# Optimization experiments

Hardware: AMD Instinct MI355X
Metric: run time of the kernel (lower is better)

Reference implementation:

```python
import jax, jax.numpy as jnp
import numpy as np

N = 1048576  # batch elements; each element is a 64-bit FP64 value stored as {0,1} float bits


def _xor(a, b):
    return a + b - 2.0 * a * b


def _mux(s, a, b):
    # s ? a : b  (spiking MUX gate)
    return s * a + (1.0 - s) * b


def _ripple_add(a, b, c0):
    """Bitwise ripple-carry add of little-endian bit vectors a,b [..., n] with carry-in c0 [...]."""
    def step(carry, ab):
        ai, bi = ab
        x = _xor(ai, bi)
        s = _xor(x, carry)
        c = ai * bi + carry * x - ai * bi * carry * x  # OR(a&b, c&(a^b))
        return c, s
    _, sums = jax.lax.scan(step, c0, (jnp.moveaxis(a, -1, 0), jnp.moveaxis(b, -1, 0)))
    return jnp.moveaxis(sums, 0, -1)


def setup_inputs() -> dict:
    key = jax.random.key(0)
    kx, kk = jax.random.split(key)
    x = jax.random.randint(kx, (N, 64), 0, 2).astype(jnp.float32)
    k = jax.random.randint(kk, (N, 64), 0, 2).astype(jnp.float32)
    return {"x": x, "k": k}


def reference(x, k):
    batch = x.shape[:-1]
    dt = x.dtype
    ones = jnp.ones(batch, dt)
    zeros = jnp.zeros(batch, dt)

    s_x = x[..., 0:1]
    e_x = x[..., 1:12]
    m_x = x[..., 12:64]
    s_k = k[..., 0:1]
    e_k = k[..., 1:12]
    m_k = k[..., 12:64]

    # shift = e_k - 1023 (little-endian, two's complement via add of NOT(1023)+1)
    e_k_le = e_k[..., ::-1]
    not_1023_le = jnp.broadcast_to(jnp.asarray([0.0] * 10 + [1.0], dt), batch + (11,))
    shift = _ripple_add(e_k_le, not_1023_le, ones)

    # barrel shifter: integer value of |k| = (1.mantissa) >> (15 - shift)  over 16 bits
    s_bar = 1.0 - shift[..., :4]  # bits of (15 - shift)
    val = jnp.concatenate([jnp.ones(batch + (1,), dt), m_k[..., :15]], axis=-1)
    current = val[..., ::-1]  # little-endian
    for layer in range(4):
        amt = 1 << layer
        shifted = jnp.concatenate([current[..., amt:], jnp.zeros(batch + (amt,), dt)], axis=-1)
        current = _mux(s_bar[..., layer:layer + 1], shifted, current)
    k_abs_le = current[..., :11]

    # negate via two's complement; select by sign of k
    neg_k = _ripple_add(1.0 - k_abs_le, jnp.zeros(batch + (11,), dt), ones)
    k_final = _mux(s_k, neg_k, k_abs_le)

    # e_new = e_x + k_final
    e_x_le = e_x[..., ::-1]
    e_new = _ripple_add(e_x_le, k_final, zeros)[..., ::-1]

    # k == 0 detection: OR-reduce bits 1..63 (OR(a,b)=1-(1-a)(1-b)), then NOT
    k_is_zero = jnp.prod(1.0 - k[..., 1:64], axis=-1, keepdims=True)

    result_scaled = jnp.concatenate([s_x, e_new, m_x], axis=-1)
    return _mux(k_is_zero, x, result_scaled)
```

## Files before the change

### kernel.cpp

```cpp
#include <hip/hip_runtime.h>


typedef unsigned int u32x4 __attribute__((ext_vector_type(4)));

__global__ __launch_bounds__(256) void spike_fp64_scale_kernel(
    const u32x4* __restrict__ x4,
    const u32x4* __restrict__ k4,
    u32x4* __restrict__ o4,
    int ntiles)
{
    const int nwaves = (int)((gridDim.x * blockDim.x) >> 6);
    const int wid    = (int)((blockIdx.x * blockDim.x + threadIdx.x) >> 6);
    const int lane   = (int)(threadIdx.x & 63);
    const int g      = lane >> 4;
    const int j      = lane & 15;

    if (wid >= ntiles) return;

    size_t idx        = (size_t)wid * 64 + lane;
    const size_t step = (size_t)nwaves * 64;

    u32x4 xv = x4[idx];
    u32x4 kv = k4[idx];

    int tile = wid;
    for (;;) {
        const int  nxt      = tile + nwaves;
        const bool has_next = nxt < ntiles;
        u32x4 xn, kn;
        if (has_next) {
            xn = x4[idx + step];
            kn = k4[idx + step];
        }

        const unsigned nx = ((xv[0] >> 23) & 1u) | ((xv[1] >> 22) & 2u)
                          | ((xv[2] >> 21) & 4u) | ((xv[3] >> 20) & 8u);
        const unsigned nk = ((kv[0] >> 23) & 1u) | ((kv[1] >> 22) & 2u)
                          | ((kv[2] >> 21) & 4u) | ((kv[3] >> 20) & 8u);

        const unsigned sh4 = (unsigned)(j & 7) * 4u;
        unsigned uxl = (j < 8) ? (nx << sh4) : 0u;
        unsigned ukl = (j < 8) ? (nk << sh4) : 0u;

        const unsigned nkm = nk & ((j == 0) ? 0xEu : 0xFu);
        const unsigned long long bal = __ballot(nkm != 0u);
        const bool kany = ((unsigned)((bal >> (g * 16)) & 0xFFFFull)) != 0u;

        #pragma unroll
        for (int m = 1; m <= 8; m <<= 1) {
            uxl |= (unsigned)__shfl_xor((int)uxl, m, 64);
            ukl |= (unsigned)__shfl_xor((int)ukl, m, 64);
        }

        const unsigned bk    = __builtin_bitreverse32(ukl);
        const unsigned ek    = (bk >> 20) & 0x7FFu;
        const unsigned val16 = 0x8000u | ((bk >> 5) & 0x7FFFu);
        const unsigned shv   = (ek + 1u) & 15u;
        const unsigned kabs  = (val16 >> (15u - shv)) & 0x7FFu;
        const unsigned kfin  = (ukl & 1u) ? ((0u - kabs) & 0x7FFu) : kabs;
        const unsigned ex    = (__builtin_bitreverse32(uxl) >> 20) & 0x7FFu;
        const unsigned enew  = (ex + kfin) & 0x7FFu;

        u32x4 o;
        const int e0 = 4 * j;
        #pragma unroll
        for (int c = 0; c < 4; ++c) {
            const int e = e0 + c;
            const unsigned bit  = (enew >> (((unsigned)(11 - e)) & 31u)) & 1u;
            const bool     repl = kany && (e >= 1) && (e <= 11);
            o[c] = repl ? (bit ? 0x3F800000u : 0u) : xv[c];
        }
        __builtin_nontemporal_store(o, &o4[idx]);

        if (!has_next) break;
        tile = nxt;
        idx += step;
        xv = xn;
        kv = kn;
    }
}

extern "C" void kernel_launch(void* const* d_in, const int* in_sizes, int n_in,
                              void* d_out, int out_size, void* d_ws, size_t ws_size,
                              hipStream_t stream) {
    const u32x4* x4 = (const u32x4*)d_in[0];
    const u32x4* k4 = (const u32x4*)d_in[1];
    u32x4* o4 = (u32x4*)d_out;

    const int nrows  = in_sizes[0] / 64;
    const int ntiles = nrows / 4;

    const int threads = 256;
    int blocks = 2048;
    const int max_blocks = (ntiles * 64 + threads - 1) / threads;
    if (blocks > max_blocks) blocks = max_blocks;

    spike_fp64_scale_kernel<<<blocks, threads, 0, stream>>>(x4, k4, o4, ntiles);
}
```

Measured before the change: 602.2 us.

## Replace grid-stride prefetch loop with one-tile-per-wave launch and DPP reductions

After: 564.3 us. -6.3%, faster.

```diff
diff --git a/kernel.cpp b/kernel.cpp
--- a/kernel.cpp
+++ b/kernel.cpp
@@ -3,81 +3,59 @@
 
 typedef unsigned int u32x4 __attribute__((ext_vector_type(4)));
 
+#define DPP_OR(v, ctrl) \
+    (v | (unsigned)__builtin_amdgcn_update_dpp(0, (int)(v), (ctrl), 0xF, 0xF, true))
+
 __global__ __launch_bounds__(256) void spike_fp64_scale_kernel(
     const u32x4* __restrict__ x4,
     const u32x4* __restrict__ k4,
-    u32x4* __restrict__ o4,
-    int ntiles)
+    u32x4* __restrict__ o4)
 {
-    const int nwaves = (int)((gridDim.x * blockDim.x) >> 6);
-    const int wid    = (int)((blockIdx.x * blockDim.x + threadIdx.x) >> 6);
-    const int lane   = (int)(threadIdx.x & 63);
-    const int g      = lane >> 4;
-    const int j      = lane & 15;
+    const int lane = (int)(threadIdx.x & 63);
+    const int g    = lane >> 4;
+    const int j    = lane & 15;
 
-    if (wid >= ntiles) return;
+    const size_t idx = (size_t)((blockIdx.x * blockDim.x + threadIdx.x) >> 6) * 64 + lane;
+    const u32x4 xv = x4[idx];
+    const u32x4 kv = k4[idx];
 
-    size_t idx        = (size_t)wid * 64 + lane;
-    const size_t step = (size_t)nwaves * 64;
+    const unsigned nx = ((xv[0] >> 23) & 1u) | ((xv[1] >> 22) & 2u)
+                      | ((xv[2] >> 21) & 4u) | ((xv[3] >> 20) & 8u);
+    const unsigned nk = ((kv[0] >> 23) & 1u) | ((kv[1] >> 22) & 2u)
+                      | ((kv[2] >> 21) & 4u) | ((kv[3] >> 20) & 8u);
 
-    u32x4 xv = x4[idx];
-    u32x4 kv = k4[idx];
+    const unsigned sh4 = (unsigned)(j & 7) * 4u;
+    unsigned uxl = (j < 8) ? (nx << sh4) : 0u;
+    unsigned ukl = (j < 8) ? (nk << sh4) : 0u;
 
-    int tile = wid;
-    for (;;) {
-        const int  nxt      = tile + nwaves;
-        const bool has_next = nxt < ntiles;
-        u32x4 xn, kn;
-        if (has_next) {
-            xn = x4[idx + step];
-            kn = k4[idx + step];
-        }
+    const unsigned nkm = nk & ((j == 0) ? 0xEu : 0xFu);
+    const unsigned long long bal = __ballot(nkm != 0u);
+    const bool kany = ((unsigned)((bal >> (g * 16)) & 0xFFFFull)) != 0u;
 
-        const unsigned nx = ((xv[0] >> 23) & 1u) | ((xv[1] >> 22) & 2u)
-                          | ((xv[2] >> 21) & 4u) | ((xv[3] >> 20) & 8u);
-        const unsigned nk = ((kv[0] >> 23) & 1u) | ((kv[1] >> 22) & 2u)
-                          | ((kv[2] >> 21) & 4u) | ((kv[3] >> 20) & 8u);
+    uxl = DPP_OR(uxl, 0xB1);  ukl = DPP_OR(ukl, 0xB1);
+    uxl = DPP_OR(uxl, 0x4E);  ukl = DPP_OR(ukl, 0x4E);
+    uxl = DPP_OR(uxl, 0x141); ukl = DPP_OR(ukl, 0x141);
+    uxl = DPP_OR(uxl, 0x140); ukl = DPP_OR(ukl, 0x140);
 
-        const unsigned sh4 = (unsigned)(j & 7) * 4u;
-        unsigned uxl = (j < 8) ? (nx << sh4) : 0u;
-        unsigned ukl = (j < 8) ? (nk << sh4) : 0u;
+    const unsigned bk    = __builtin_bitreverse32(ukl);
+    const unsigned ek    = (bk >> 20) & 0x7FFu;
+    const unsigned val16 = 0x8000u | ((bk >> 5) & 0x7FFFu);
+    const unsigned shv   = (ek + 1u) & 15u;
+    const unsigned kabs  = (val16 >> (15u - shv)) & 0x7FFu;
+    const unsigned kfin  = (ukl & 1u) ? ((0u - kabs) & 0x7FFu) : kabs;
+    const unsigned ex    = (__builtin_bitreverse32(uxl) >> 20) & 0x7FFu;
+    const unsigned enew  = (ex + kfin) & 0x7FFu;
 
-        const unsigned nkm = nk & ((j == 0) ? 0xEu : 0xFu);
-        const unsigned long long bal = __ballot(nkm != 0u);
-        const bool kany = ((unsigned)((bal >> (g * 16)) & 0xFFFFull)) != 0u;
-
-        #pragma unroll
-        for (int m = 1; m <= 8; m <<= 1) {
-            uxl |= (unsigned)__shfl_xor((int)uxl, m, 64);
-            ukl |= (unsigned)__shfl_xor((int)ukl, m, 64);
-        }
-
-        const unsigned bk    = __builtin_bitreverse32(ukl);
-        const unsigned ek    = (bk >> 20) & 0x7FFu;
-        const unsigned val16 = 0x8000u | ((bk >> 5) & 0x7FFFu);
-        const unsigned shv   = (ek + 1u) & 15u;
-        const unsigned kabs  = (val16 >> (15u - shv)) & 0x7FFu;
-        const unsigned kfin  = (ukl & 1u) ? ((0u - kabs) & 0x7FFu) : kabs;
-        const unsigned ex    = (__builtin_bitreverse32(uxl) >> 20) & 0x7FFu;
-        const unsigned enew  = (ex + kfin) & 0x7FFu;
-
-        u32x4 o;
-        const int e0 = 4 * j;
-        #pragma unroll
-        for (int c = 0; c < 4; ++c) {
-            const int e = e0 + c;
-            const unsigned bit  = (enew >> (((unsigned)(11 - e)) & 31u)) & 1u;
-            const bool     repl = kany && (e >= 1) && (e <= 11);
-            o[c] = repl ? (bit ? 0x3F800000u : 0u) : xv[c];
-        }
-        __builtin_nontemporal_store(o, &o4[idx]);
-
-        if (!has_next) break;
-        tile = nxt;
-        idx += step;
-        xv = xn;
-        kv = kn;
+    u32x4 o;
+    const int e0 = 4 * j;
+    #pragma unroll
+    for (int c = 0; c < 4; ++c) {
+        const int e = e0 + c;
+        const unsigned bit  = (enew >> (((unsigned)(11 - e)) & 31u)) & 1u;
+        const bool     repl = kany && (e >= 1) && (e <= 11);
+        o[c] = repl ? (bit ? 0x3F800000u : 0u) : xv[c];
     }
+    o4[idx] = o;
 }
 
 extern "C" void kernel_launch(void* const* d_in, const int* in_sizes, int n_in,
@@ -87,13 +65,10 @@
     const u32x4* k4 = (const u32x4*)d_in[1];
     u32x4* o4 = (u32x4*)d_out;
 
-    const int nrows  = in_sizes[0] / 64;
-    const int ntiles = nrows / 4;
+    const int nrows = in_sizes[0] / 64;
+    const int total_threads = nrows * 16;
+    const int threads = 256;
+    const int blocks = total_threads / threads;
 
-    const int threads = 256;
-    int blocks = 2048;
-    const int max_blocks = (ntiles * 64 + threads - 1) / threads;
-    if (blocks > max_blocks) blocks = max_blocks;
-
-    spike_fp64_scale_kernel<<<blocks, threads, 0, stream>>>(x4, k4, o4, ntiles);
+    spike_fp64_scale_kernel<<<blocks, threads, 0, stream>>>(x4, k4, o4);
 }
```
